# Kernel tuning notes

Hardware: AMD Instinct MI355X
Metric: run time of the kernel (lower is better)

The kernel has to match this reference:

```python
import jax, jax.numpy as jnp
import numpy as np

NEG_SLOPE = 0.2


def gat_conv(x, src, dst, W, att_src, att_dst, bias, heads, out_ch):
    # x: [N, Fin]; src/dst: [E] (self-loops already included)
    N = x.shape[0]
    h = (x @ W).reshape(N, heads, out_ch)                      # [N, H, C]
    a_s = jnp.einsum('nhc,hc->nh', h, att_src)                 # [N, H]
    a_d = jnp.einsum('nhc,hc->nh', h, att_dst)                 # [N, H]
    e = jax.nn.leaky_relu(a_s[src] + a_d[dst], NEG_SLOPE)      # [E, H]
    # segment softmax over incoming edges of each dst node
    e_max = jax.ops.segment_max(e, dst, num_segments=N)        # [N, H]
    p = jnp.exp(e - e_max[dst])                                # [E, H]
    denom = jax.ops.segment_sum(p, dst, num_segments=N)        # [N, H]
    alpha = p / denom[dst]                                     # [E, H]
    msg = h[src] * alpha[:, :, None]                           # [E, H, C]
    out = jax.ops.segment_sum(msg, dst, num_segments=N)        # [N, H, C]
    return out.reshape(N, heads * out_ch) + bias


def setup_inputs() -> dict:
    key = jax.random.key(0)
    ks = jax.random.split(key, 10)
    N, E, F_IN, HID, HEADS, NCLS = 100000, 3200000, 512, 8, 8, 16
    x = jax.random.normal(ks[0], (N, F_IN), dtype=jnp.float32)
    edge_index = jax.random.randint(ks[1], (2, E), 0, N, dtype=jnp.int64)
    s = 1.0 / np.sqrt(F_IN)
    W1 = jax.random.uniform(ks[2], (F_IN, HEADS * HID), jnp.float32, -s, s)
    att_src1 = jax.random.normal(ks[3], (HEADS, HID), jnp.float32) * 0.1
    att_dst1 = jax.random.normal(ks[4], (HEADS, HID), jnp.float32) * 0.1
    b1 = jnp.zeros((HEADS * HID,), jnp.float32)
    s2 = 1.0 / np.sqrt(HEADS * HID)
    W2 = jax.random.uniform(ks[5], (HEADS * HID, NCLS), jnp.float32, -s2, s2)
    att_src2 = jax.random.normal(ks[6], (1, NCLS), jnp.float32) * 0.1
    att_dst2 = jax.random.normal(ks[7], (1, NCLS), jnp.float32) * 0.1
    b2 = jnp.zeros((NCLS,), jnp.float32)
    return {"x": x, "edge_index": edge_index, "W1": W1, "att_src1": att_src1,
            "att_dst1": att_dst1, "b1": b1, "W2": W2, "att_src2": att_src2,
            "att_dst2": att_dst2, "b2": b2}


def reference(x, edge_index, W1, att_src1, att_dst1, b1, W2, att_src2, att_dst2, b2):
    N = x.shape[0]
    loops = jnp.arange(N, dtype=edge_index.dtype)
    src = jnp.concatenate([edge_index[0], loops])  # PyG add_self_loops=True
    dst = jnp.concatenate([edge_index[1], loops])
    # eval mode: F.dropout is identity
    h = gat_conv(x, src, dst, W1, att_src1, att_dst1, b1, heads=8, out_ch=8)
    h = jax.nn.elu(h)
    out = gat_conv(h, src, dst, W2, att_src2, att_dst2, b2, heads=1, out_ch=16)
    return out
```

## Files before the change

kernel.cpp:

```cpp
#include <hip/hip_runtime.h>
#include <hip/hip_fp16.h>

#define F_IN 512
#define F1 64
#define NCLS 16
#define NEG_SLOPE 0.2f

typedef __attribute__((ext_vector_type(8))) short short8;
typedef __attribute__((ext_vector_type(4))) float f32x4;

__device__ __forceinline__ unsigned short f2bf(float f) {
    unsigned u = __float_as_uint(f);
    return (unsigned short)((u + 0x7fffu + ((u >> 16) & 1u)) >> 16);
}
__device__ __forceinline__ float bf2f(unsigned short u) {
    return __uint_as_float(((unsigned)u) << 16);
}


__global__ __launch_bounds__(64) void k_detect(const int* __restrict__ ei, int E,
                                               unsigned* __restrict__ mode) {
    int t = threadIdx.x;
    unsigned nz = 0;
    int lim = (E > 256) ? 256 : E;
    for (int k = t; k < lim; k += 64) nz |= (unsigned)ei[2 * k + 1];
    for (int off = 1; off < 64; off <<= 1) nz |= __shfl_xor(nz, off);
    if (t == 0) *mode = (nz == 0) ? 1u : 0u;
}

__device__ __forceinline__ void decode_edge(const int* __restrict__ ei,
                                            const long long* __restrict__ e64,
                                            bool m64, unsigned i, int E, int N,
                                            int& s, int& v) {
    if (i < (unsigned)E) {
        if (m64) { s = (int)e64[i]; v = (int)e64[E + i]; }
        else     { s = ei[i];       v = ei[E + i]; }
    } else {
        s = (int)(i - (unsigned)E);
        v = s;
    }
    s = s < 0 ? 0 : (s >= N ? N - 1 : s);
    v = v < 0 ? 0 : (v >= N ? N - 1 : v);
}

__device__ __forceinline__ int decode_dst(const int* __restrict__ ei,
                                          const long long* __restrict__ e64,
                                          bool m64, unsigned i, int E, int N) {
    int v;
    if (i < (unsigned)E) v = m64 ? (int)e64[E + i] : ei[E + i];
    else                 v = (int)(i - (unsigned)E);
    return v < 0 ? 0 : (v >= N ? N - 1 : v);
}


__global__ __launch_bounds__(256) void k_prep(const float* __restrict__ W1,
                                              unsigned short* __restrict__ W1T) {
    int t = blockIdx.x * 256 + threadIdx.x;
    if (t < F_IN * F1) {
        int k = t >> 6, c = t & 63;
        W1T[(size_t)c * F_IN + k] = f2bf(W1[t]);
    }
}


__device__ __forceinline__ void gemm1_tile(const float* __restrict__ x,
                                           const unsigned short* __restrict__ W1T,
                                           const float* __restrict__ att_s,
                                           const float* __restrict__ att_d,
                                           unsigned short* __restrict__ h1b,
                                           __half* __restrict__ a_s1,
                                           float* __restrict__ a_d1,
                                           int N, int row0, char* sm) {
    const int tid = threadIdx.x;
    const int w = tid >> 6, lane = tid & 63;
    const int quad = lane >> 4, r16 = lane & 15;

    f32x4 acc[4];
#pragma unroll
    for (int t = 0; t < 4; t++) acc[t] = (f32x4){0.f, 0.f, 0.f, 0.f};

    const int a_row = tid >> 2;
    const int a_seg = (tid & 3) * 8;
    const int b_col = tid & 63;
    const int b_kq  = tid >> 6;
    const int ar = row0 + a_row;
    const bool arok = ar < N;
    const float* xrow = x + (size_t)ar * F_IN + a_seg;
    const unsigned short* wrow = W1T + (size_t)b_col * F_IN + b_kq * 8;

    float4 v0 = make_float4(0.f, 0.f, 0.f, 0.f), v1 = v0;
    short8 rb;
    if (arok) { v0 = *(const float4*)(xrow); v1 = *(const float4*)(xrow + 4); }
    rb = *(const short8*)(wrow);
    {
        unsigned short (*A)[40] = (unsigned short (*)[40])(sm);
        unsigned short (*B)[40] = (unsigned short (*)[40])(sm + 5120);
        short8 cv;
        cv[0] = (short)f2bf(v0.x); cv[1] = (short)f2bf(v0.y);
        cv[2] = (short)f2bf(v0.z); cv[3] = (short)f2bf(v0.w);
        cv[4] = (short)f2bf(v1.x); cv[5] = (short)f2bf(v1.y);
        cv[6] = (short)f2bf(v1.z); cv[7] = (short)f2bf(v1.w);
        *(short8*)&A[a_row][a_seg] = cv;
        *(short8*)&B[b_col][b_kq * 8] = rb;
    }
    __syncthreads();

    int cur = 0;
#pragma unroll
    for (int k = 0; k < F_IN / 32; k++) {
        if (k + 1 < F_IN / 32) {
            v0 = make_float4(0.f, 0.f, 0.f, 0.f); v1 = v0;
            if (arok) {
                const float* xp = xrow + (k + 1) * 32;
                v0 = *(const float4*)xp; v1 = *(const float4*)(xp + 4);
            }
            rb = *(const short8*)(wrow + (k + 1) * 32);
        }
        {
            unsigned short (*A)[40] = (unsigned short (*)[40])(sm + cur * 10240);
            unsigned short (*B)[40] = (unsigned short (*)[40])(sm + cur * 10240 + 5120);
            short8 af = *(const short8*)&A[w * 16 + r16][quad * 8];
#pragma unroll
            for (int t = 0; t < 4; t++) {
                short8 bf = *(const short8*)&B[t * 16 + r16][quad * 8];
                acc[t] = __builtin_amdgcn_mfma_f32_16x16x32_bf16(af, bf, acc[t], 0, 0, 0);
            }
        }
        if (k + 1 < F_IN / 32) {
            unsigned short (*A)[40] = (unsigned short (*)[40])(sm + (cur ^ 1) * 10240);
            unsigned short (*B)[40] = (unsigned short (*)[40])(sm + (cur ^ 1) * 10240 + 5120);
            short8 cv;
            cv[0] = (short)f2bf(v0.x); cv[1] = (short)f2bf(v0.y);
            cv[2] = (short)f2bf(v0.z); cv[3] = (short)f2bf(v0.w);
            cv[4] = (short)f2bf(v1.x); cv[5] = (short)f2bf(v1.y);
            cv[6] = (short)f2bf(v1.z); cv[7] = (short)f2bf(v1.w);
            *(short8*)&A[a_row][a_seg] = cv;
            *(short8*)&B[b_col][b_kq * 8] = rb;
        }
        __syncthreads();
        cur ^= 1;
    }

    float ats[4], atd[4];
#pragma unroll
    for (int t = 0; t < 4; t++) {
        ats[t] = att_s[t * 16 + r16];
        atd[t] = att_d[t * 16 + r16];
    }
#pragma unroll
    for (int r = 0; r < 4; r++) {
        int grow = row0 + w * 16 + quad * 4 + r;
        bool ok = grow < N;
        float ps[4], pd[4];
#pragma unroll
        for (int t = 0; t < 4; t++) {
            float vv = acc[t][r];
            if (ok) h1b[(size_t)grow * F1 + t * 16 + r16] = f2bf(vv);
            ps[t] = vv * ats[t];
            pd[t] = vv * atd[t];
        }
#pragma unroll
        for (int t = 0; t < 4; t++) {
            ps[t] += __shfl_xor(ps[t], 1); pd[t] += __shfl_xor(pd[t], 1);
            ps[t] += __shfl_xor(ps[t], 2); pd[t] += __shfl_xor(pd[t], 2);
            ps[t] += __shfl_xor(ps[t], 4); pd[t] += __shfl_xor(pd[t], 4);
        }
        if (ok && (r16 & 7) == 0) {
            int hh0 = r16 >> 3;
#pragma unroll
            for (int t = 0; t < 4; t++) {
                a_s1[(size_t)grow * 8 + t * 2 + hh0] = __float2half_rn(ps[t]);
                a_d1[(size_t)grow * 8 + t * 2 + hh0] = pd[t];
            }
        }
    }
}


__global__ __launch_bounds__(256) void k_fusedA(const float* __restrict__ x,
                                                const unsigned short* __restrict__ W1T,
                                                const float* __restrict__ att_s,
                                                const float* __restrict__ att_d,
                                                unsigned short* __restrict__ h1b,
                                                __half* __restrict__ a_s1,
                                                float* __restrict__ a_d1, int N,
                                                const int* __restrict__ ei,
                                                const unsigned* __restrict__ mode,
                                                unsigned* __restrict__ bucketCnt,
                                                int E, int ET, int nch,
                                                int nb, int shift) {
    __shared__ __align__(16) char smem[20480];
    unsigned b = blockIdx.x;
    if ((b & 1) == 0) {
        gemm1_tile(x, W1T, att_s, att_d, h1b, a_s1, a_d1, N, (int)(b >> 1) * 64, smem);
        return;
    }
    unsigned* cntL = (unsigned*)smem;
    for (int i = threadIdx.x; i < 1024; i += 256) cntL[i] = 0u;
    __syncthreads();

    const unsigned stride = (unsigned)nch * 256u;
    bool m64 = (*mode != 0u);
    const long long* e64 = (const long long*)ei;
    unsigned i = (b >> 1) * 256u + threadIdx.x;
    for (; i + 3u * stride < (unsigned)ET; i += 4u * stride) {
        int v0 = decode_dst(ei, e64, m64, i, E, N);
        int v1 = decode_dst(ei, e64, m64, i + stride, E, N);
        int v2 = decode_dst(ei, e64, m64, i + 2u * stride, E, N);
        int v3 = decode_dst(ei, e64, m64, i + 3u * stride, E, N);
        atomicAdd(&cntL[(unsigned)v0 >> shift], 1u);
        atomicAdd(&cntL[(unsigned)v1 >> shift], 1u);
        atomicAdd(&cntL[(unsigned)v2 >> shift], 1u);
        atomicAdd(&cntL[(unsigned)v3 >> shift], 1u);
    }
    for (; i < (unsigned)ET; i += stride) {
        int v = decode_dst(ei, e64, m64, i, E, N);
        atomicAdd(&cntL[(unsigned)v >> shift], 1u);
    }
    __syncthreads();
    for (int k = threadIdx.x; k < nb; k += 256) {
        unsigned c = cntL[k];
        if (c) atomicAdd(&bucketCnt[k], c);
    }
}


__global__ __launch_bounds__(256) void k_fusedB(const float* __restrict__ x,
                                                const unsigned short* __restrict__ W1T,
                                                const float* __restrict__ att_s,
                                                const float* __restrict__ att_d,
                                                unsigned short* __restrict__ h1b,
                                                __half* __restrict__ a_s1,
                                                float* __restrict__ a_d1, int N,
                                                int rowSplit,
                                                const int* __restrict__ ei,
                                                const unsigned* __restrict__ mode,
                                                unsigned* __restrict__ bucketFill,
                                                unsigned* __restrict__ pairs,
                                                int E, int ET, int nch,
                                                int nb, int shift) {
    __shared__ __align__(16) char smem[20480];
    unsigned b = blockIdx.x;
    if (b & 1) {
        gemm1_tile(x, W1T, att_s, att_d, h1b, a_s1, a_d1, N,
                   rowSplit + (int)(b >> 1) * 64, smem);
        return;
    }
    unsigned* cntA = (unsigned*)smem;
    unsigned* ofsA = (unsigned*)(smem + 4096);
    unsigned* part = (unsigned*)(smem + 8192);
    const int t = threadIdx.x;
    const int chunk = (ET + nch - 1) / nch;
    const int cbase = (int)(b >> 1) * chunk;
    const int cend = (cbase + chunk < ET) ? cbase + chunk : ET;
    const unsigned lmask = (1u << shift) - 1u;
    bool m64 = (*mode != 0u);
    const long long* e64 = (const long long*)ei;

    for (int k = t; k < 1024; k += 256) cntA[k] = 0u;
    __syncthreads();
    for (int k = cbase + t; k < cend; k += 256) {
        int v = decode_dst(ei, e64, m64, (unsigned)k, E, N);
        atomicAdd(&cntA[(unsigned)v >> shift], 1u);
    }
    __syncthreads();
    unsigned a0 = cntA[4 * t + 0], a1 = cntA[4 * t + 1];
    unsigned a2 = cntA[4 * t + 2], a3 = cntA[4 * t + 3];
    unsigned ssum = a0 + a1 + a2 + a3;
    part[t] = ssum;
    __syncthreads();
    for (int off = 1; off < 256; off <<= 1) {
        unsigned add = (t >= off) ? part[t - off] : 0u;
        __syncthreads();
        part[t] += add;
        __syncthreads();
    }
    unsigned excl = part[t] - ssum;
    ofsA[4 * t + 0] = excl;
    ofsA[4 * t + 1] = excl + a0;
    ofsA[4 * t + 2] = excl + a0 + a1;
    ofsA[4 * t + 3] = excl + a0 + a1 + a2;
    __syncthreads();
    for (int k = t; k < nb; k += 256) {
        unsigned c = cntA[k];
        unsigned g = c ? atomicAdd(&bucketFill[k], c) : 0u;
        cntA[k] = g - ofsA[k];
    }
    __syncthreads();
    for (int k = cbase + t; k < cend; k += 256) {
        int s, v;
        decode_edge(ei, e64, m64, (unsigned)k, E, N, s, v);
        unsigned bb = (unsigned)v >> shift;
        unsigned slot = atomicAdd(&ofsA[bb], 1u);
        pairs[cntA[bb] + slot] = (unsigned)s | (((unsigned)v & lmask) << 20);
    }
}


__global__ __launch_bounds__(1024) void k_scan_buckets(const unsigned* __restrict__ bucketCnt,
                                                       int nb, int ET,
                                                       unsigned* __restrict__ bucketOfs,
                                                       unsigned* __restrict__ bucketFill,
                                                       unsigned* __restrict__ row_ptr,
                                                       int N) {
    __shared__ unsigned sbuf[1024];
    int t = threadIdx.x;
    unsigned val = (t < nb) ? bucketCnt[t] : 0u;
    sbuf[t] = val;
    __syncthreads();
    for (int off = 1; off < 1024; off <<= 1) {
        unsigned add = (t >= off) ? sbuf[t - off] : 0u;
        __syncthreads();
        sbuf[t] += add;
        __syncthreads();
    }
    if (t < nb) {
        unsigned e = sbuf[t] - val;
        bucketOfs[t] = e;
        bucketFill[t] = e;
    }
    if (t == 0) row_ptr[N] = (unsigned)ET;
}


__global__ __launch_bounds__(256) void k_sort(const unsigned* __restrict__ pairs,
                                              const unsigned* __restrict__ bucketOfs,
                                              const unsigned* __restrict__ bucketCnt,
                                              unsigned* __restrict__ row_ptr,
                                              unsigned* __restrict__ ssrc,
                                              int N, int shift) {
    __shared__ unsigned f[1024];
    __shared__ unsigned part[256];
    const int b = blockIdx.x;
    const int t = threadIdx.x;
    const int nodes = 1 << shift;
    const int bbase = b << shift;
    for (int i = t; i < 1024; i += 256) f[i] = 0u;
    __syncthreads();
    const unsigned base = bucketOfs[b];
    const unsigned cnt = bucketCnt[b];
    for (unsigned i = (unsigned)t; i < cnt; i += 256u)
        atomicAdd(&f[pairs[base + i] >> 20], 1u);
    __syncthreads();
    unsigned a0 = f[4 * t + 0], a1 = f[4 * t + 1];
    unsigned a2 = f[4 * t + 2], a3 = f[4 * t + 3];
    unsigned ssum = a0 + a1 + a2 + a3;
    part[t] = ssum;
    __syncthreads();
    for (int off = 1; off < 256; off <<= 1) {
        unsigned add = (t >= off) ? part[t - off] : 0u;
        __syncthreads();
        part[t] += add;
        __syncthreads();
    }
    unsigned excl = part[t] - ssum;
    unsigned c0 = base + excl;
    unsigned c1 = c0 + a0;
    unsigned c2 = c1 + a1;
    unsigned c3 = c2 + a2;
    {
        int v0 = bbase + 4 * t;
        if (v0 + 0 < N && 4 * t + 0 < nodes) row_ptr[v0 + 0] = c0;
        if (v0 + 1 < N && 4 * t + 1 < nodes) row_ptr[v0 + 1] = c1;
        if (v0 + 2 < N && 4 * t + 2 < nodes) row_ptr[v0 + 2] = c2;
        if (v0 + 3 < N && 4 * t + 3 < nodes) row_ptr[v0 + 3] = c3;
    }
    f[4 * t + 0] = c0;
    f[4 * t + 1] = c1;
    f[4 * t + 2] = c2;
    f[4 * t + 3] = c3;
    __syncthreads();
    for (unsigned i = (unsigned)t; i < cnt; i += 256u) {
        unsigned pk = pairs[base + i];
        unsigned local = pk >> 20;
        unsigned pos = atomicAdd(&f[local], 1u);
        ssrc[pos] = pk & 0xFFFFFu;
    }
}


__global__ __launch_bounds__(256) void k_agg1(const unsigned short* __restrict__ h1b,
                                              const __half* __restrict__ a_s1,
                                              const float* __restrict__ a_d1,
                                              const float* __restrict__ b1,
                                              const unsigned* __restrict__ row_ptr,
                                              const unsigned* __restrict__ ssrc,
                                              float* __restrict__ g, int N) {
    int wid = threadIdx.x >> 6, lane = threadIdx.x & 63;
    int v = blockIdx.x * 4 + wid;
    if (v >= N) return;
    unsigned base = row_ptr[v];
    unsigned deg = row_ptr[v + 1] - base;

    const int eA = lane >> 3, hA = lane & 7;
    float adv = a_d1[(size_t)v * 8 + hA];
    const int half = lane >> 5, j32 = lane & 31;
    const int hq = j32 >> 2;

    float denom = 0.f, acc0 = 0.f, acc1 = 0.f;
    for (unsigned jj = 0; jj < deg; jj += 8) {
        unsigned ee = jj + (unsigned)eA;
        bool val = ee < deg;
        unsigned sL = ssrc[base + (val ? ee : 0u)];
        float as = __half2float(a_s1[(size_t)sL * 8 + hA]);
        float eatt = as + adv;
        eatt = eatt > 0.f ? eatt : NEG_SLOPE * eatt;
        float p = val ? __expf(eatt) : 0.f;
        denom += p;
#pragma unroll
        for (int k = 0; k < 4; k++) {
            int esel = k * 2 + half;
            unsigned s_my = (unsigned)__shfl((int)sL, esel * 8);
            float p_my = __shfl(p, esel * 8 + hq);
            unsigned u = *(const unsigned*)(h1b + ((size_t)s_my << 6) + (j32 << 1));
            float lo = __uint_as_float(u << 16);
            float hi = __uint_as_float(u & 0xffff0000u);
            acc0 = fmaf(lo, p_my, acc0);
            acc1 = fmaf(hi, p_my, acc1);
        }
    }
    acc0 += __shfl_xor(acc0, 32);
    acc1 += __shfl_xor(acc1, 32);
    denom += __shfl_xor(denom, 8);
    denom += __shfl_xor(denom, 16);
    denom += __shfl_xor(denom, 32);
    float dn = __shfl(denom, hq);
    if (half == 0) {
        float inv = 1.0f / dn;
        int c0 = j32 * 2;
        float t0 = acc0 * inv + b1[c0];
        float t1 = acc1 * inv + b1[c0 + 1];
        t0 = t0 > 0.f ? t0 : (__expf(t0) - 1.f);
        t1 = t1 > 0.f ? t1 : (__expf(t1) - 1.f);
        *(float2*)&g[(size_t)v * F1 + c0] = make_float2(t0, t1);
    }
}


__global__ __launch_bounds__(256) void k_gemm2(const float* __restrict__ g,
                                               const float* __restrict__ W2,
                                               const float* __restrict__ as2w,
                                               const float* __restrict__ ad2w,
                                               __half* __restrict__ h2,
                                               float* __restrict__ a_s2,
                                               float* __restrict__ a_d2, int N) {
    __shared__ float W2s[F1][NCLS];
    int tid = threadIdx.x;
    for (int i = tid; i < F1 * NCLS; i += 256) ((float*)W2s)[i] = W2[i];
    __syncthreads();
    int lane = tid & 63, wid = tid >> 6;
    int n = blockIdx.x * 16 + wid * 4 + (lane >> 4);
    int c = lane & 15;
    if (n >= N) return;
    float acc = 0.f;
#pragma unroll
    for (int k4 = 0; k4 < 16; k4++) {
        float4 gv = *(const float4*)(g + (size_t)n * F1 + k4 * 4);
        acc = fmaf(gv.x, W2s[k4 * 4 + 0][c], acc);
        acc = fmaf(gv.y, W2s[k4 * 4 + 1][c], acc);
        acc = fmaf(gv.z, W2s[k4 * 4 + 2][c], acc);
        acc = fmaf(gv.w, W2s[k4 * 4 + 3][c], acc);
    }
    h2[(size_t)n * NCLS + c] = __float2half_rn(acc);
    float s = acc * as2w[c];
    float d = acc * ad2w[c];
    s += __shfl_xor(s, 1); s += __shfl_xor(s, 2); s += __shfl_xor(s, 4); s += __shfl_xor(s, 8);
    d += __shfl_xor(d, 1); d += __shfl_xor(d, 2); d += __shfl_xor(d, 4); d += __shfl_xor(d, 8);
    if (c == 0) { a_s2[n] = s; a_d2[n] = d; }
}


__global__ __launch_bounds__(256) void k_agg2(const __half* __restrict__ h2,
                                              const float* __restrict__ a_s2,
                                              const float* __restrict__ a_d2,
                                              const float* __restrict__ b2,
                                              const unsigned* __restrict__ row_ptr,
                                              const unsigned* __restrict__ ssrc,
                                              float* __restrict__ out, int N) {
    int wid = threadIdx.x >> 6, lane = threadIdx.x & 63;
    int v = blockIdx.x * 4 + wid;
    if (v >= N) return;
    unsigned base = row_ptr[v];
    unsigned deg = row_ptr[v + 1] - base;
    float adv = a_d2[v];
    int sub = lane >> 4, c = lane & 15;

    float denom = 0.f, acc = 0.f;
    unsigned j = sub;
    for (; j + 12 < deg; j += 16) {
        unsigned s0 = ssrc[base + j + 0];
        unsigned s1 = ssrc[base + j + 4];
        unsigned s2 = ssrc[base + j + 8];
        unsigned s3 = ssrc[base + j + 12];
        float as0 = a_s2[s0];
        float as1 = a_s2[s1];
        float as2 = a_s2[s2];
        float as3 = a_s2[s3];
        float h0 = __half2float(h2[(size_t)s0 * NCLS + c]);
        float h1v = __half2float(h2[(size_t)s1 * NCLS + c]);
        float h2v = __half2float(h2[(size_t)s2 * NCLS + c]);
        float h3 = __half2float(h2[(size_t)s3 * NCLS + c]);
        float e0 = as0 + adv; e0 = e0 > 0.f ? e0 : NEG_SLOPE * e0; float p0 = __expf(e0);
        float e1 = as1 + adv; e1 = e1 > 0.f ? e1 : NEG_SLOPE * e1; float p1 = __expf(e1);
        float e2 = as2 + adv; e2 = e2 > 0.f ? e2 : NEG_SLOPE * e2; float p2 = __expf(e2);
        float e3 = as3 + adv; e3 = e3 > 0.f ? e3 : NEG_SLOPE * e3; float p3 = __expf(e3);
        denom += (p0 + p1) + (p2 + p3);
        acc = fmaf(h0, p0, acc);
        acc = fmaf(h1v, p1, acc);
        acc = fmaf(h2v, p2, acc);
        acc = fmaf(h3, p3, acc);
    }
    for (; j < deg; j += 4) {
        unsigned s = ssrc[base + j];
        float as = a_s2[s];
        float hv = __half2float(h2[(size_t)s * NCLS + c]);
        float e = as + adv; e = e > 0.f ? e : NEG_SLOPE * e;
        float p = __expf(e);
        denom += p;
        acc = fmaf(hv, p, acc);
    }
    acc += __shfl_xor(acc, 16);
    acc += __shfl_xor(acc, 32);
    denom += __shfl_xor(denom, 16);
    denom += __shfl_xor(denom, 32);
    if (lane < 16) {
        out[(size_t)v * NCLS + c] = acc * (1.0f / denom) + b2[c];
    }
}


static inline size_t algn(size_t x) { return (x + 255) & ~(size_t)255; }

extern "C" void kernel_launch(void* const* d_in, const int* in_sizes, int n_in,
                              void* d_out, int out_size, void* d_ws, size_t ws_size,
                              hipStream_t stream) {
    const float* x   = (const float*)d_in[0];
    const int* ei    = (const int*)d_in[1];
    const float* W1  = (const float*)d_in[2];
    const float* as1 = (const float*)d_in[3];
    const float* ad1 = (const float*)d_in[4];
    const float* b1  = (const float*)d_in[5];
    const float* W2  = (const float*)d_in[6];
    const float* as2 = (const float*)d_in[7];
    const float* ad2 = (const float*)d_in[8];
    const float* b2  = (const float*)d_in[9];

    const int N = in_sizes[0] / F_IN;
    const int E = in_sizes[1] / 2;
    const int ET = E + N;

    int shift = 8;
    int nb = (N + 255) >> 8;
    while (nb > 1024) { shift++; nb = (N + (1 << shift) - 1) >> shift; }

    const int GA_T = ((N / 2) + 63) / 64;
    const int rowSplit = GA_T * 64;
    const int GB_T = (N - rowSplit + 63) / 64;

    char* p = (char*)d_ws;
    unsigned short* h1b = (unsigned short*)p;  p += algn((size_t)N * F1 * 2);
    float* g    = (float*)p;      p += algn((size_t)N * F1 * 4);
    __half* a_s1 = (__half*)p;    p += algn((size_t)N * 8 * 2);
    float* a_d1 = (float*)p;      p += algn((size_t)N * 8 * 4);
    __half* h2  = (__half*)p;     p += algn((size_t)N * NCLS * 2);
    float* a_s2 = (float*)p;      p += algn((size_t)N * 4);
    float* a_d2 = (float*)p;      p += algn((size_t)N * 4);
    unsigned* row_ptr = (unsigned*)p;  p += algn((size_t)(N + 1) * 4);
    unsigned* bucketCnt  = (unsigned*)p;  p += algn((size_t)1024 * 4);
    unsigned* bucketOfs  = (unsigned*)p;  p += algn((size_t)1024 * 4);
    unsigned* bucketFill = (unsigned*)p;  p += algn((size_t)1024 * 4);
    unsigned* mode    = (unsigned*)p;  p += algn(256);
    unsigned short* W1T = (unsigned short*)p;  p += algn((size_t)F_IN * F1 * 2);
    unsigned* ssrc = (unsigned*)p;     p += algn((size_t)ET * 4);
    unsigned* pairs = (unsigned*)g;

    hipMemsetAsync(bucketCnt, 0, (size_t)nb * 4, stream);

    dim3 b256(256);
    k_detect<<<dim3(1), dim3(64), 0, stream>>>(ei, E, mode);
    k_prep<<<dim3((F_IN * F1 + 255) / 256), b256, 0, stream>>>(W1, W1T);

    k_fusedA<<<dim3(2 * GA_T), b256, 0, stream>>>(x, W1T, as1, ad1, h1b, a_s1, a_d1, N,
                                                  ei, mode, bucketCnt,
                                                  E, ET, GA_T, nb, shift);

    k_scan_buckets<<<dim3(1), dim3(1024), 0, stream>>>(bucketCnt, nb, ET, bucketOfs,
                                                       bucketFill, row_ptr, N);

    k_fusedB<<<dim3(2 * GB_T), b256, 0, stream>>>(x, W1T, as1, ad1, h1b, a_s1, a_d1, N,
                                                  rowSplit, ei, mode, bucketFill,
                                                  pairs, E, ET, GB_T, nb, shift);

    k_sort<<<dim3(nb), b256, 0, stream>>>(pairs, bucketOfs, bucketCnt, row_ptr, ssrc, N, shift);

    k_agg1<<<dim3((N + 3) / 4), b256, 0, stream>>>(h1b, a_s1, a_d1, b1, row_ptr, ssrc, g, N);
    k_gemm2<<<dim3((N + 15) / 16), b256, 0, stream>>>(g, W2, as2, ad2, h2, a_s2, a_d2, N);
    k_agg2<<<dim3((N + 3) / 4), b256, 0, stream>>>(h2, a_s2, a_d2, b2, row_ptr, ssrc,
                                                   (float*)d_out, N);
}
```

Before: 596.7 us.

## Load GEMM1 operands directly into registers and decouple sort-block count from GEMM tiles

The GEMM1 tile no longer stages x and W1T through double-buffered LDS with barriers. Each wave now loads its A fragment from global memory, converts it to bf16 in registers, and reads B fragments straight from the L2-resident W1T. The fused kernels also switch from interleaving even/odd blocks to a fixed 256 counting/scatter blocks followed by GEMM blocks, with contiguous edge chunks per block. This cuts LDS use and syncs, which should raise occupancy, but adds redundant global W1T reads across waves and fewer sort blocks than before.

Result: faster. 571.4 us (-4.2%).

```diff
diff --git a/kernel.cpp b/kernel.cpp
--- a/kernel.cpp
+++ b/kernel.cpp
@@ -5,6 +5,7 @@
 #define F1 64
 #define NCLS 16
 #define NEG_SLOPE 0.2f
+#define NS 256
 
 typedef __attribute__((ext_vector_type(8))) short short8;
 typedef __attribute__((ext_vector_type(4))) float f32x4;
@@ -70,7 +71,7 @@
                                            unsigned short* __restrict__ h1b,
                                            __half* __restrict__ a_s1,
                                            float* __restrict__ a_d1,
-                                           int N, int row0, char* sm) {
+                                           int N, int row0) {
     const int tid = threadIdx.x;
     const int w = tid >> 6, lane = tid & 63;
     const int quad = lane >> 4, r16 = lane & 15;
@@ -79,66 +80,30 @@
 #pragma unroll
     for (int t = 0; t < 4; t++) acc[t] = (f32x4){0.f, 0.f, 0.f, 0.f};
 
-    const int a_row = tid >> 2;
-    const int a_seg = (tid & 3) * 8;
-    const int b_col = tid & 63;
-    const int b_kq  = tid >> 6;
-    const int ar = row0 + a_row;
-    const bool arok = ar < N;
-    const float* xrow = x + (size_t)ar * F_IN + a_seg;
-    const unsigned short* wrow = W1T + (size_t)b_col * F_IN + b_kq * 8;
-
-    float4 v0 = make_float4(0.f, 0.f, 0.f, 0.f), v1 = v0;
-    short8 rb;
-    if (arok) { v0 = *(const float4*)(xrow); v1 = *(const float4*)(xrow + 4); }
-    rb = *(const short8*)(wrow);
-    {
-        unsigned short (*A)[40] = (unsigned short (*)[40])(sm);
-        unsigned short (*B)[40] = (unsigned short (*)[40])(sm + 5120);
-        short8 cv;
-        cv[0] = (short)f2bf(v0.x); cv[1] = (short)f2bf(v0.y);
-        cv[2] = (short)f2bf(v0.z); cv[3] = (short)f2bf(v0.w);
-        cv[4] = (short)f2bf(v1.x); cv[5] = (short)f2bf(v1.y);
-        cv[6] = (short)f2bf(v1.z); cv[7] = (short)f2bf(v1.w);
-        *(short8*)&A[a_row][a_seg] = cv;
-        *(short8*)&B[b_col][b_kq * 8] = rb;
-    }
-    __syncthreads();
-
-    int cur = 0;
-#pragma unroll
-    for (int k = 0; k < F_IN / 32; k++) {
-        if (k + 1 < F_IN / 32) {
-            v0 = make_float4(0.f, 0.f, 0.f, 0.f); v1 = v0;
-            if (arok) {
-                const float* xp = xrow + (k + 1) * 32;
-                v0 = *(const float4*)xp; v1 = *(const float4*)(xp + 4);
+    const int arow = row0 + w * 16 + r16;
+    const bool rok = arow < N;
+    const float* xrow = x + (size_t)arow * F_IN + quad * 8;
+    const unsigned short* wbase = W1T + quad * 8;
+
+#pragma unroll 4
+    for (int k0 = 0; k0 < F_IN; k0 += 32) {
+        short8 af;
+        {
+            float4 v0 = make_float4(0.f, 0.f, 0.f, 0.f), v1 = v0;
+            if (rok) {
+                v0 = *(const float4*)(xrow + k0);
+                v1 = *(const float4*)(xrow + k0 + 4);
             }
-            rb = *(const short8*)(wrow + (k + 1) * 32);
+            af[0] = (short)f2bf(v0.x); af[1] = (short)f2bf(v0.y);
+            af[2] = (short)f2bf(v0.z); af[3] = (short)f2bf(v0.w);
+            af[4] = (short)f2bf(v1.x); af[5] = (short)f2bf(v1.y);
+            af[6] = (short)f2bf(v1.z); af[7] = (short)f2bf(v1.w);
         }
-        {
-            unsigned short (*A)[40] = (unsigned short (*)[40])(sm + cur * 10240);
-            unsigned short (*B)[40] = (unsigned short (*)[40])(sm + cur * 10240 + 5120);
-            short8 af = *(const short8*)&A[w * 16 + r16][quad * 8];
-#pragma unroll
-            for (int t = 0; t < 4; t++) {
-                short8 bf = *(const short8*)&B[t * 16 + r16][quad * 8];
-                acc[t] = __builtin_amdgcn_mfma_f32_16x16x32_bf16(af, bf, acc[t], 0, 0, 0);
-            }
+#pragma unroll
+        for (int t = 0; t < 4; t++) {
+            short8 bf = *(const short8*)(wbase + (size_t)(t * 16 + r16) * F_IN + k0);
+            acc[t] = __builtin_amdgcn_mfma_f32_16x16x32_bf16(af, bf, acc[t], 0, 0, 0);
         }
-        if (k + 1 < F_IN / 32) {
-            unsigned short (*A)[40] = (unsigned short (*)[40])(sm + (cur ^ 1) * 10240);
-            unsigned short (*B)[40] = (unsigned short (*)[40])(sm + (cur ^ 1) * 10240 + 5120);
-            short8 cv;
-            cv[0] = (short)f2bf(v0.x); cv[1] = (short)f2bf(v0.y);
-            cv[2] = (short)f2bf(v0.z); cv[3] = (short)f2bf(v0.w);
-            cv[4] = (short)f2bf(v1.x); cv[5] = (short)f2bf(v1.y);
-            cv[6] = (short)f2bf(v1.z); cv[7] = (short)f2bf(v1.w);
-            *(short8*)&A[a_row][a_seg] = cv;
-            *(short8*)&B[b_col][b_kq * 8] = rb;
-        }
-        __syncthreads();
-        cur ^= 1;
     }
 
     float ats[4], atd[4];
@@ -187,34 +152,35 @@
                                                 const int* __restrict__ ei,
                                                 const unsigned* __restrict__ mode,
                                                 unsigned* __restrict__ bucketCnt,
-                                                int E, int ET, int nch,
+                                                int E, int ET,
                                                 int nb, int shift) {
-    __shared__ __align__(16) char smem[20480];
+    __shared__ unsigned cntL[1024];
     unsigned b = blockIdx.x;
-    if ((b & 1) == 0) {
-        gemm1_tile(x, W1T, att_s, att_d, h1b, a_s1, a_d1, N, (int)(b >> 1) * 64, smem);
+    if (b >= NS) {
+        gemm1_tile(x, W1T, att_s, att_d, h1b, a_s1, a_d1, N, (int)(b - NS) * 64);
         return;
     }
-    unsigned* cntL = (unsigned*)smem;
     for (int i = threadIdx.x; i < 1024; i += 256) cntL[i] = 0u;
     __syncthreads();
 
-    const unsigned stride = (unsigned)nch * 256u;
+    const int chunk = (ET + NS - 1) / NS;
+    const int cbase = (int)b * chunk;
+    const int cend = (cbase + chunk < ET) ? cbase + chunk : ET;
     bool m64 = (*mode != 0u);
     const long long* e64 = (const long long*)ei;
-    unsigned i = (b >> 1) * 256u + threadIdx.x;
-    for (; i + 3u * stride < (unsigned)ET; i += 4u * stride) {
-        int v0 = decode_dst(ei, e64, m64, i, E, N);
-        int v1 = decode_dst(ei, e64, m64, i + stride, E, N);
-        int v2 = decode_dst(ei, e64, m64, i + 2u * stride, E, N);
-        int v3 = decode_dst(ei, e64, m64, i + 3u * stride, E, N);
+    int i = cbase + threadIdx.x;
+    for (; i + 768 < cend; i += 1024) {
+        int v0 = decode_dst(ei, e64, m64, (unsigned)i, E, N);
+        int v1 = decode_dst(ei, e64, m64, (unsigned)(i + 256), E, N);
+        int v2 = decode_dst(ei, e64, m64, (unsigned)(i + 512), E, N);
+        int v3 = decode_dst(ei, e64, m64, (unsigned)(i + 768), E, N);
         atomicAdd(&cntL[(unsigned)v0 >> shift], 1u);
         atomicAdd(&cntL[(unsigned)v1 >> shift], 1u);
         atomicAdd(&cntL[(unsigned)v2 >> shift], 1u);
         atomicAdd(&cntL[(unsigned)v3 >> shift], 1u);
     }
-    for (; i < (unsigned)ET; i += stride) {
-        int v = decode_dst(ei, e64, m64, i, E, N);
+    for (; i < cend; i += 256) {
+        int v = decode_dst(ei, e64, m64, (unsigned)i, E, N);
         atomicAdd(&cntL[(unsigned)v >> shift], 1u);
     }
     __syncthreads();
@@ -237,21 +203,20 @@
                                                 const unsigned* __restrict__ mode,
                                                 unsigned* __restrict__ bucketFill,
                                                 unsigned* __restrict__ pairs,
-                                                int E, int ET, int nch,
+                                                int E, int ET,
                                                 int nb, int shift) {
-    __shared__ __align__(16) char smem[20480];
+    __shared__ unsigned cntA[1024];
+    __shared__ unsigned ofsA[1024];
+    __shared__ unsigned part[256];
     unsigned b = blockIdx.x;
-    if (b & 1) {
+    if (b >= NS) {
         gemm1_tile(x, W1T, att_s, att_d, h1b, a_s1, a_d1, N,
-                   rowSplit + (int)(b >> 1) * 64, smem);
+                   rowSplit + (int)(b - NS) * 64);
         return;
     }
-    unsigned* cntA = (unsigned*)smem;
-    unsigned* ofsA = (unsigned*)(smem + 4096);
-    unsigned* part = (unsigned*)(smem + 8192);
     const int t = threadIdx.x;
-    const int chunk = (ET + nch - 1) / nch;
-    const int cbase = (int)(b >> 1) * chunk;
+    const int chunk = (ET + NS - 1) / NS;
+    const int cbase = (int)b * chunk;
     const int cend = (cbase + chunk < ET) ? cbase + chunk : ET;
     const unsigned lmask = (1u << shift) - 1u;
     bool m64 = (*mode != 0u);
@@ -580,16 +545,16 @@
     k_detect<<<dim3(1), dim3(64), 0, stream>>>(ei, E, mode);
     k_prep<<<dim3((F_IN * F1 + 255) / 256), b256, 0, stream>>>(W1, W1T);
 
-    k_fusedA<<<dim3(2 * GA_T), b256, 0, stream>>>(x, W1T, as1, ad1, h1b, a_s1, a_d1, N,
-                                                  ei, mode, bucketCnt,
-                                                  E, ET, GA_T, nb, shift);
+    k_fusedA<<<dim3(NS + GA_T), b256, 0, stream>>>(x, W1T, as1, ad1, h1b, a_s1, a_d1, N,
+                                                   ei, mode, bucketCnt,
+                                                   E, ET, nb, shift);
 
     k_scan_buckets<<<dim3(1), dim3(1024), 0, stream>>>(bucketCnt, nb, ET, bucketOfs,
                                                        bucketFill, row_ptr, N);
 
-    k_fusedB<<<dim3(2 * GB_T), b256, 0, stream>>>(x, W1T, as1, ad1, h1b, a_s1, a_d1, N,
-                                                  rowSplit, ei, mode, bucketFill,
-                                                  pairs, E, ET, GB_T, nb, shift);
+    k_fusedB<<<dim3(NS + GB_T), b256, 0, stream>>>(x, W1T, as1, ad1, h1b, a_s1, a_d1, N,
+                                                   rowSplit, ei, mode, bucketFill,
+                                                   pairs, E, ET, nb, shift);
 
     k_sort<<<dim3(nb), b256, 0, stream>>>(pairs, bucketOfs, bucketCnt, row_ptr, ssrc, N, shift);
 
```
